# Optimization experiments

Hardware: AMD Instinct MI355X
Metric: run time of the kernel (lower is better)

## Reference

```python
import jax, jax.numpy as jnp
import numpy as np

B, H, W, D, K = 64, 32, 32, 512, 64
EPS = 1e-12


def setup_inputs() -> dict:
    key = jax.random.key(0)
    k1, k2, k3 = jax.random.split(key, 3)
    inputs = jax.random.normal(k1, (B, H, W, D), dtype=jnp.float32)
    # 1x1 conv kernel (no bias) -> equivalent to a [D, K] matmul per pixel
    w = jax.random.normal(k2, (D, K), dtype=jnp.float32) * 0.02
    # cluster centers, stored in the original as (1,1,1,D,K); we keep [D, K]
    C = jax.random.normal(k3, (D, K), dtype=jnp.float32) * 0.02
    return {"inputs": inputs, "w": w, "C": C}


def _l2norm(v, axis=-1):
    return v / jnp.sqrt(jnp.sum(v * v, axis=axis, keepdims=True) + EPS)


def reference(inputs, w, C):
    # soft-assignment: 1x1 conv + softmax over clusters
    s = jnp.einsum('bhwd,dk->bhwk', inputs, w)          # [B,H,W,K]
    a = jax.nn.softmax(s, axis=-1)
    b, h, ww, d = inputs.shape
    k = w.shape[1]
    a2 = a.reshape(b, h * ww, k)                         # [B,N,K]
    x2 = inputs.reshape(b, h * ww, d)                    # [B,N,D]
    # VLAD reformulation: sum_n a[n,k]*(x[n,d] + C[d,k])
    #  = (a^T x)[k,d] + (sum_n a[n,k]) * C[d,k]
    # avoids materializing the [B,H,W,D,K] broadcast of the original
    vkd = jnp.einsum('bnk,bnd->bkd', a2, x2)             # [B,K,D]
    vkd = vkd + a2.sum(axis=1)[:, :, None] * C.T[None]   # [B,K,D]
    # intra-normalization over D (matches transpose->normalize in original)
    vkd = _l2norm(vkd, axis=-1)
    # transpose back to [B,D,K], flatten, global L2 normalize
    v = jnp.transpose(vkd, (0, 2, 1)).reshape(b, d * k)
    v = _l2norm(v, axis=-1)
    return v
```

## Files before the change

### kernel.cpp

```cpp
#include <hip/hip_runtime.h>

#define EPS 1e-12f
typedef __attribute__((ext_vector_type(8))) short short8;
typedef __attribute__((ext_vector_type(4))) float f32x4;

__device__ __forceinline__ unsigned short f2bf(float f) {
  unsigned u = __float_as_uint(f);
  u += 0x7FFFu + ((u >> 16) & 1u);
  return (unsigned short)(u >> 16);
}
__device__ __forceinline__ float bf2f(unsigned short h) {
  return __uint_as_float(((unsigned)h) << 16);
}
__device__ __forceinline__ void split2(float f, unsigned short& h,
                                       unsigned short& l) {
  h = f2bf(f);
  l = f2bf(f - bf2f(h));
}

extern "C" __global__ __launch_bounds__(256) void netvlad_prep(
    const float* __restrict__ w, unsigned short* __restrict__ wTh,
    unsigned short* __restrict__ wTl)
{
  int tg = blockIdx.x * 256 + threadIdx.x;
  int k = tg >> 9, d = tg & 511;
  float f = w[d * 64 + k];
  unsigned short h, l;
  split2(f, h, l);
  wTh[tg] = h;
  wTl[tg] = l;
}

extern "C" __global__ __launch_bounds__(256) void netvlad_assign(
    const float* __restrict__ x, const unsigned short* __restrict__ wTh,
    const unsigned short* __restrict__ wTl, unsigned short* __restrict__ aTh,
    unsigned short* __restrict__ aTl, float* __restrict__ asum)
{
  __shared__ unsigned short xh[64 * 40];
  __shared__ unsigned short xl[64 * 40];
  __shared__ unsigned short ath[64 * 80];
  __shared__ unsigned short atl[64 * 80];
  __shared__ float asp[4 * 64];

  const int t = threadIdx.x;
  const int lane = t & 63, wv = t >> 6;
  const int lo4 = lane & 15, hi4 = lane >> 4;
  const int pxblk = blockIdx.x << 6;
  const int b = blockIdx.x >> 4;
  const int nblk = (blockIdx.x & 15) << 6;

  f32x4 acc[4] = {{0.f, 0.f, 0.f, 0.f}, {0.f, 0.f, 0.f, 0.f},
                  {0.f, 0.f, 0.f, 0.f}, {0.f, 0.f, 0.f, 0.f}};

  const int spx = t >> 2;
  const int sd = (t & 3) * 8;
  const float* xrow = x + (size_t)(pxblk + spx) * 512 + sd;

  for (int d0 = 0; d0 < 512; d0 += 32) {
    __syncthreads();
    float4 v0 = *(const float4*)(xrow + d0);
    float4 v1 = *(const float4*)(xrow + d0 + 4);
    ushort4 h0, h1, l0, l1;
    split2(v0.x, h0.x, l0.x); split2(v0.y, h0.y, l0.y);
    split2(v0.z, h0.z, l0.z); split2(v0.w, h0.w, l0.w);
    split2(v1.x, h1.x, l1.x); split2(v1.y, h1.y, l1.y);
    split2(v1.z, h1.z, l1.z); split2(v1.w, h1.w, l1.w);
    *(ushort4*)&xh[spx * 40 + sd] = h0;
    *(ushort4*)&xh[spx * 40 + sd + 4] = h1;
    *(ushort4*)&xl[spx * 40 + sd] = l0;
    *(ushort4*)&xl[spx * 40 + sd + 4] = l1;
    __syncthreads();

    short8 xfh = *(short8*)&xh[(wv * 16 + lo4) * 40 + hi4 * 8];
    short8 xfl = *(short8*)&xl[(wv * 16 + lo4) * 40 + hi4 * 8];
#pragma unroll
    for (int nt = 0; nt < 4; ++nt) {
      const size_t wo = (size_t)(nt * 16 + lo4) * 512 + d0 + hi4 * 8;
      short8 wfh = *(const short8*)(wTh + wo);
      short8 wfl = *(const short8*)(wTl + wo);
      acc[nt] = __builtin_amdgcn_mfma_f32_16x16x32_bf16(xfh, wfh, acc[nt], 0, 0, 0);
      acc[nt] = __builtin_amdgcn_mfma_f32_16x16x32_bf16(xfl, wfh, acc[nt], 0, 0, 0);
      acc[nt] = __builtin_amdgcn_mfma_f32_16x16x32_bf16(xfh, wfl, acc[nt], 0, 0, 0);
    }
  }

  float asum_p[4] = {0.f, 0.f, 0.f, 0.f};
#pragma unroll
  for (int r = 0; r < 4; ++r) {
    float s0 = acc[0][r], s1 = acc[1][r], s2 = acc[2][r], s3 = acc[3][r];
    float m = fmaxf(fmaxf(s0, s1), fmaxf(s2, s3));
    m = fmaxf(m, __shfl_xor(m, 1));
    m = fmaxf(m, __shfl_xor(m, 2));
    m = fmaxf(m, __shfl_xor(m, 4));
    m = fmaxf(m, __shfl_xor(m, 8));
    float e0 = __expf(s0 - m), e1 = __expf(s1 - m);
    float e2 = __expf(s2 - m), e3 = __expf(s3 - m);
    float s = e0 + e1 + e2 + e3;
    s += __shfl_xor(s, 1);
    s += __shfl_xor(s, 2);
    s += __shfl_xor(s, 4);
    s += __shfl_xor(s, 8);
    float inv = 1.0f / s;
    e0 *= inv; e1 *= inv; e2 *= inv; e3 *= inv;
    asum_p[0] += e0; asum_p[1] += e1; asum_p[2] += e2; asum_p[3] += e3;
    const int px = wv * 16 + hi4 * 4 + r;
    unsigned short h, l;
    split2(e0, h, l); ath[(0 * 16 + lo4) * 80 + px] = h; atl[(0 * 16 + lo4) * 80 + px] = l;
    split2(e1, h, l); ath[(1 * 16 + lo4) * 80 + px] = h; atl[(1 * 16 + lo4) * 80 + px] = l;
    split2(e2, h, l); ath[(2 * 16 + lo4) * 80 + px] = h; atl[(2 * 16 + lo4) * 80 + px] = l;
    split2(e3, h, l); ath[(3 * 16 + lo4) * 80 + px] = h; atl[(3 * 16 + lo4) * 80 + px] = l;
  }
#pragma unroll
  for (int nt = 0; nt < 4; ++nt) {
    float v = asum_p[nt];
    v += __shfl_xor(v, 16);
    v += __shfl_xor(v, 32);
    if (lane < 16) asp[wv * 64 + nt * 16 + lane] = v;
  }
  __syncthreads();
  if (t < 64) {
    float s = asp[t] + asp[64 + t] + asp[128 + t] + asp[192 + t];
    atomicAdd(&asum[b * 64 + t], s);
  }
  {
    const int k = t >> 2, po = (t & 3) * 16;
    short8 h0 = *(short8*)&ath[k * 80 + po];
    short8 h1 = *(short8*)&ath[k * 80 + po + 8];
    short8 l0 = *(short8*)&atl[k * 80 + po];
    short8 l1 = *(short8*)&atl[k * 80 + po + 8];
    const size_t go = ((size_t)(b * 64 + k) << 10) + nblk + po;
    *(short8*)(aTh + go) = h0;
    *(short8*)(aTh + go + 8) = h1;
    *(short8*)(aTl + go) = l0;
    *(short8*)(aTl + go + 8) = l1;
  }
}

extern "C" __global__ __launch_bounds__(256) void netvlad_vlad(
    const float* __restrict__ x, const unsigned short* __restrict__ aTh,
    const unsigned short* __restrict__ aTl, float* __restrict__ vkd)
{
  __shared__ unsigned short xth[32 * 40];
  __shared__ unsigned short xtl[32 * 40];
  const int t = threadIdx.x;
  const int lane = t & 63, wv = t >> 6;
  const int lo4 = lane & 15, hi4 = lane >> 4;
  const int b = blockIdx.x >> 4;
  const int ds = (blockIdx.x & 15) << 5;
  const int np = (t & 15) * 2;
  const int sdd = (t >> 4) * 2;
  const float* xs = x + (size_t)b * 1024 * 512 + ds;

  f32x4 acc[2] = {{0.f, 0.f, 0.f, 0.f}, {0.f, 0.f, 0.f, 0.f}};

  for (int n0 = 0; n0 < 1024; n0 += 32) {
    __syncthreads();
    float2 u = *(const float2*)(xs + (size_t)(n0 + np) * 512 + sdd);
    float2 v = *(const float2*)(xs + (size_t)(n0 + np + 1) * 512 + sdd);
    ushort2 h0, h1, l0, l1;
    split2(u.x, h0.x, l0.x); split2(v.x, h0.y, l0.y);
    split2(u.y, h1.x, l1.x); split2(v.y, h1.y, l1.y);
    *(ushort2*)&xth[sdd * 40 + np] = h0;
    *(ushort2*)&xth[(sdd + 1) * 40 + np] = h1;
    *(ushort2*)&xtl[sdd * 40 + np] = l0;
    *(ushort2*)&xtl[(sdd + 1) * 40 + np] = l1;
    __syncthreads();

    const size_t ao = (size_t)(b * 64 + wv * 16 + lo4) * 1024 + n0 + hi4 * 8;
    short8 ah = *(const short8*)(aTh + ao);
    short8 al = *(const short8*)(aTl + ao);
#pragma unroll
    for (int dt = 0; dt < 2; ++dt) {
      short8 bh = *(short8*)&xth[(dt * 16 + lo4) * 40 + hi4 * 8];
      short8 bl = *(short8*)&xtl[(dt * 16 + lo4) * 40 + hi4 * 8];
      acc[dt] = __builtin_amdgcn_mfma_f32_16x16x32_bf16(ah, bh, acc[dt], 0, 0, 0);
      acc[dt] = __builtin_amdgcn_mfma_f32_16x16x32_bf16(ah, bl, acc[dt], 0, 0, 0);
      acc[dt] = __builtin_amdgcn_mfma_f32_16x16x32_bf16(al, bh, acc[dt], 0, 0, 0);
    }
  }
#pragma unroll
  for (int dt = 0; dt < 2; ++dt) {
    float* vb = vkd + ((size_t)(b * 512 + ds + dt * 16 + lo4)) * 64
              + wv * 16 + hi4 * 4;
    *(float4*)vb = make_float4(acc[dt][0], acc[dt][1], acc[dt][2], acc[dt][3]);
  }
}

extern "C" __global__ __launch_bounds__(256) void netvlad_fin1(
    const float* __restrict__ vkd, const float* __restrict__ Cm,
    const float* __restrict__ asum, float* __restrict__ out,
    float* __restrict__ r_buf)
{
  __shared__ float rp[4 * 64];
  const int t = threadIdx.x;
  const int k = t & 63;
  const int dg = t >> 6;
  const int b = blockIdx.x >> 2;
  const int dq = blockIdx.x & 3;
  const float asv = asum[b * 64 + k];
  const int dbase = dq * 128 + dg * 32;
  const float* p0 = vkd + (size_t)b * 512 * 64;
  float* ob = out + (size_t)b * 512 * 64;
  float racc = 0.f;
  for (int dd = 0; dd < 32; ++dd) {
    size_t off = (size_t)(dbase + dd) * 64 + k;
    float v = p0[off] + asv * Cm[off];
    ob[off] = v;
    racc = fmaf(v, v, racc);
  }
  rp[dg * 64 + k] = racc;
  __syncthreads();
  if (t < 64) {
    float r = rp[t] + rp[64 + t] + rp[128 + t] + rp[192 + t];
    atomicAdd(&r_buf[b * 64 + t], r);
  }
}

extern "C" __global__ __launch_bounds__(64) void netvlad_fin2(
    const float* __restrict__ r_buf, float* __restrict__ scale_buf)
{
  const int b = blockIdx.x;
  const int k = threadIdx.x;
  float r = r_buf[b * 64 + k];
  float g = r / (r + EPS);
  g += __shfl_xor(g, 1);
  g += __shfl_xor(g, 2);
  g += __shfl_xor(g, 4);
  g += __shfl_xor(g, 8);
  g += __shfl_xor(g, 16);
  g += __shfl_xor(g, 32);
  scale_buf[b * 64 + k] = 1.0f / (sqrtf(r + EPS) * sqrtf(g + EPS));
}

extern "C" __global__ __launch_bounds__(256) void netvlad_fin3(
    float* __restrict__ out, const float* __restrict__ scale_buf)
{
  __shared__ float sc[64];
  const int t = threadIdx.x;
  const int b = blockIdx.x >> 3;
  if (t < 64) sc[t] = scale_buf[b * 64 + t];
  __syncthreads();
  float4* o4 = (float4*)out;
#pragma unroll
  for (int c = 0; c < 4; ++c) {
    int idx = blockIdx.x * 1024 + c * 256 + t;
    float4 v = o4[idx];
    int k4 = (idx & 15) * 4;
    v.x *= sc[k4]; v.y *= sc[k4 + 1]; v.z *= sc[k4 + 2]; v.w *= sc[k4 + 3];
    o4[idx] = v;
  }
}

extern "C" void kernel_launch(void* const* d_in, const int* in_sizes, int n_in,
                              void* d_out, int out_size, void* d_ws,
                              size_t ws_size, hipStream_t stream)
{
  const float* x  = (const float*)d_in[0];
  const float* w  = (const float*)d_in[1];
  const float* Cm = (const float*)d_in[2];
  float* out = (float*)d_out;

  unsigned short* aTh = (unsigned short*)d_ws;
  unsigned short* aTl = aTh + 4194304;
  float* vkd = (float*)(aTl + 4194304);
  unsigned short* wTh = (unsigned short*)(vkd + 2097152);
  unsigned short* wTl = wTh + 32768;
  float* asum = (float*)(wTl + 32768);
  float* r_buf = asum + 4096;
  float* scale_buf = r_buf + 4096;

  hipMemsetAsync(asum, 0, 2 * 4096 * sizeof(float), stream);

  netvlad_prep  <<< 128, 256, 0, stream>>>(w, wTh, wTl);
  netvlad_assign<<<1024, 256, 0, stream>>>(x, wTh, wTl, aTh, aTl, asum);
  netvlad_vlad  <<<1024, 256, 0, stream>>>(x, aTh, aTl, vkd);
  netvlad_fin1  <<< 256, 256, 0, stream>>>(vkd, Cm, asum, out, r_buf);
  netvlad_fin2  <<<  64,  64, 0, stream>>>(r_buf, scale_buf);
  netvlad_fin3  <<< 512, 256, 0, stream>>>(out, scale_buf);
}
```

Measured before the change: 306.0 us.

## Enlarge assign and vlad tiles, load x fragments directly, stage fp32 x in LDS

The assign kernel now handles 128 pixels per block. Each wave loads its x fragments straight from global memory into registers, with no LDS staging and no barriers in the K loop, and reuses each W fragment across two pixel tiles. The vlad kernel now covers 64 d-columns per block and all 64 clusters per wave. It stages raw fp32 x in LDS and does the bf16 hi/lo split after a transposed read, reusing each split x fragment across four cluster tiles. This halves the grid sizes and raises register pressure and LDS bank-conflict risk, in exchange for fewer barriers and more reuse of each loaded operand.

```diff
diff --git a/kernel.cpp b/kernel.cpp
--- a/kernel.cpp
+++ b/kernel.cpp
@@ -4,18 +4,37 @@
 typedef __attribute__((ext_vector_type(8))) short short8;
 typedef __attribute__((ext_vector_type(4))) float f32x4;
 
-__device__ __forceinline__ unsigned short f2bf(float f) {
-  unsigned u = __float_as_uint(f);
-  u += 0x7FFFu + ((u >> 16) & 1u);
-  return (unsigned short)(u >> 16);
-}
-__device__ __forceinline__ float bf2f(unsigned short h) {
-  return __uint_as_float(((unsigned)h) << 16);
-}
-__device__ __forceinline__ void split2(float f, unsigned short& h,
-                                       unsigned short& l) {
-  h = f2bf(f);
-  l = f2bf(f - bf2f(h));
+#define MFMA(a, b, c) __builtin_amdgcn_mfma_f32_16x16x32_bf16(a, b, c, 0, 0, 0)
+
+__device__ __forceinline__ unsigned rne16(unsigned u) {
+  return u + 0x7FFFu + ((u >> 16) & 1u);
+}
+__device__ __forceinline__ void split_pair(float f0, float f1,
+                                           unsigned& hp, unsigned& lp) {
+  unsigned u0 = __float_as_uint(f0), u1 = __float_as_uint(f1);
+  unsigned r0 = rne16(u0), r1 = rne16(u1);
+  float h0 = __uint_as_float(r0 & 0xFFFF0000u);
+  float h1 = __uint_as_float(r1 & 0xFFFF0000u);
+  hp = (r0 >> 16) | (r1 & 0xFFFF0000u);
+  unsigned v0 = rne16(__float_as_uint(f0 - h0));
+  unsigned v1 = rne16(__float_as_uint(f1 - h1));
+  lp = (v0 >> 16) | (v1 & 0xFFFF0000u);
+}
+__device__ __forceinline__ void split8(float4 a, float4 b, short8& h, short8& l) {
+  union { unsigned u[4]; short8 s; } H, L;
+  split_pair(a.x, a.y, H.u[0], L.u[0]);
+  split_pair(a.z, a.w, H.u[1], L.u[1]);
+  split_pair(b.x, b.y, H.u[2], L.u[2]);
+  split_pair(b.z, b.w, H.u[3], L.u[3]);
+  h = H.s; l = L.s;
+}
+__device__ __forceinline__ void split8f(const float* f, short8& h, short8& l) {
+  union { unsigned u[4]; short8 s; } H, L;
+  split_pair(f[0], f[1], H.u[0], L.u[0]);
+  split_pair(f[2], f[3], H.u[1], L.u[1]);
+  split_pair(f[4], f[5], H.u[2], L.u[2]);
+  split_pair(f[6], f[7], H.u[3], L.u[3]);
+  h = H.s; l = L.s;
 }
 
 extern "C" __global__ __launch_bounds__(256) void netvlad_prep(
@@ -25,10 +44,12 @@
   int tg = blockIdx.x * 256 + threadIdx.x;
   int k = tg >> 9, d = tg & 511;
   float f = w[d * 64 + k];
-  unsigned short h, l;
-  split2(f, h, l);
-  wTh[tg] = h;
-  wTl[tg] = l;
+  unsigned u = __float_as_uint(f);
+  unsigned rh = rne16(u);
+  float hf = __uint_as_float(rh & 0xFFFF0000u);
+  unsigned rl = rne16(__float_as_uint(f - hf));
+  wTh[tg] = (unsigned short)(rh >> 16);
+  wTl[tg] = (unsigned short)(rl >> 16);
 }
 
 extern "C" __global__ __launch_bounds__(256) void netvlad_assign(
@@ -36,103 +57,105 @@
     const unsigned short* __restrict__ wTl, unsigned short* __restrict__ aTh,
     unsigned short* __restrict__ aTl, float* __restrict__ asum)
 {
-  __shared__ unsigned short xh[64 * 40];
-  __shared__ unsigned short xl[64 * 40];
-  __shared__ unsigned short ath[64 * 80];
-  __shared__ unsigned short atl[64 * 80];
+  __shared__ unsigned short ath[64 * 136];
+  __shared__ unsigned short atl[64 * 136];
   __shared__ float asp[4 * 64];
 
   const int t = threadIdx.x;
   const int lane = t & 63, wv = t >> 6;
   const int lo4 = lane & 15, hi4 = lane >> 4;
-  const int pxblk = blockIdx.x << 6;
-  const int b = blockIdx.x >> 4;
-  const int nblk = (blockIdx.x & 15) << 6;
-
-  f32x4 acc[4] = {{0.f, 0.f, 0.f, 0.f}, {0.f, 0.f, 0.f, 0.f},
-                  {0.f, 0.f, 0.f, 0.f}, {0.f, 0.f, 0.f, 0.f}};
-
-  const int spx = t >> 2;
-  const int sd = (t & 3) * 8;
-  const float* xrow = x + (size_t)(pxblk + spx) * 512 + sd;
+  const int b = blockIdx.x >> 3;
+  const int nblk = (blockIdx.x & 7) << 7;
+
+  f32x4 acc[2][4] = {};
+
+  const float* xp0 =
+      x + (size_t)((blockIdx.x << 7) + (wv << 5) + lo4) * 512 + (hi4 << 3);
 
   for (int d0 = 0; d0 < 512; d0 += 32) {
-    __syncthreads();
-    float4 v0 = *(const float4*)(xrow + d0);
-    float4 v1 = *(const float4*)(xrow + d0 + 4);
-    ushort4 h0, h1, l0, l1;
-    split2(v0.x, h0.x, l0.x); split2(v0.y, h0.y, l0.y);
-    split2(v0.z, h0.z, l0.z); split2(v0.w, h0.w, l0.w);
-    split2(v1.x, h1.x, l1.x); split2(v1.y, h1.y, l1.y);
-    split2(v1.z, h1.z, l1.z); split2(v1.w, h1.w, l1.w);
-    *(ushort4*)&xh[spx * 40 + sd] = h0;
-    *(ushort4*)&xh[spx * 40 + sd + 4] = h1;
-    *(ushort4*)&xl[spx * 40 + sd] = l0;
-    *(ushort4*)&xl[spx * 40 + sd + 4] = l1;
-    __syncthreads();
-
-    short8 xfh = *(short8*)&xh[(wv * 16 + lo4) * 40 + hi4 * 8];
-    short8 xfl = *(short8*)&xl[(wv * 16 + lo4) * 40 + hi4 * 8];
+    short8 xh[2], xl[2];
+#pragma unroll
+    for (int pt = 0; pt < 2; ++pt) {
+      const float* p = xp0 + (size_t)pt * (16 * 512) + d0;
+      float4 v0 = *(const float4*)p;
+      float4 v1 = *(const float4*)(p + 4);
+      split8(v0, v1, xh[pt], xl[pt]);
+    }
 #pragma unroll
     for (int nt = 0; nt < 4; ++nt) {
-      const size_t wo = (size_t)(nt * 16 + lo4) * 512 + d0 + hi4 * 8;
-      short8 wfh = *(const short8*)(wTh + wo);
-      short8 wfl = *(const short8*)(wTl + wo);
-      acc[nt] = __builtin_amdgcn_mfma_f32_16x16x32_bf16(xfh, wfh, acc[nt], 0, 0, 0);
-      acc[nt] = __builtin_amdgcn_mfma_f32_16x16x32_bf16(xfl, wfh, acc[nt], 0, 0, 0);
-      acc[nt] = __builtin_amdgcn_mfma_f32_16x16x32_bf16(xfh, wfl, acc[nt], 0, 0, 0);
+      const size_t wo = (size_t)((nt << 4) + lo4) * 512 + d0 + (hi4 << 3);
+      short8 wh = *(const short8*)(wTh + wo);
+      short8 wl = *(const short8*)(wTl + wo);
+#pragma unroll
+      for (int pt = 0; pt < 2; ++pt) {
+        acc[pt][nt] = MFMA(xh[pt], wh, acc[pt][nt]);
+        acc[pt][nt] = MFMA(xl[pt], wh, acc[pt][nt]);
+        acc[pt][nt] = MFMA(xh[pt], wl, acc[pt][nt]);
+      }
     }
   }
 
   float asum_p[4] = {0.f, 0.f, 0.f, 0.f};
 #pragma unroll
-  for (int r = 0; r < 4; ++r) {
-    float s0 = acc[0][r], s1 = acc[1][r], s2 = acc[2][r], s3 = acc[3][r];
-    float m = fmaxf(fmaxf(s0, s1), fmaxf(s2, s3));
-    m = fmaxf(m, __shfl_xor(m, 1));
-    m = fmaxf(m, __shfl_xor(m, 2));
-    m = fmaxf(m, __shfl_xor(m, 4));
-    m = fmaxf(m, __shfl_xor(m, 8));
-    float e0 = __expf(s0 - m), e1 = __expf(s1 - m);
-    float e2 = __expf(s2 - m), e3 = __expf(s3 - m);
-    float s = e0 + e1 + e2 + e3;
-    s += __shfl_xor(s, 1);
-    s += __shfl_xor(s, 2);
-    s += __shfl_xor(s, 4);
-    s += __shfl_xor(s, 8);
-    float inv = 1.0f / s;
-    e0 *= inv; e1 *= inv; e2 *= inv; e3 *= inv;
-    asum_p[0] += e0; asum_p[1] += e1; asum_p[2] += e2; asum_p[3] += e3;
-    const int px = wv * 16 + hi4 * 4 + r;
-    unsigned short h, l;
-    split2(e0, h, l); ath[(0 * 16 + lo4) * 80 + px] = h; atl[(0 * 16 + lo4) * 80 + px] = l;
-    split2(e1, h, l); ath[(1 * 16 + lo4) * 80 + px] = h; atl[(1 * 16 + lo4) * 80 + px] = l;
-    split2(e2, h, l); ath[(2 * 16 + lo4) * 80 + px] = h; atl[(2 * 16 + lo4) * 80 + px] = l;
-    split2(e3, h, l); ath[(3 * 16 + lo4) * 80 + px] = h; atl[(3 * 16 + lo4) * 80 + px] = l;
-  }
+  for (int pt = 0; pt < 2; ++pt) {
+#pragma unroll
+    for (int r = 0; r < 4; ++r) {
+      float s0 = acc[pt][0][r], s1 = acc[pt][1][r];
+      float s2 = acc[pt][2][r], s3 = acc[pt][3][r];
+      float m = fmaxf(fmaxf(s0, s1), fmaxf(s2, s3));
+      m = fmaxf(m, __shfl_xor(m, 1));
+      m = fmaxf(m, __shfl_xor(m, 2));
+      m = fmaxf(m, __shfl_xor(m, 4));
+      m = fmaxf(m, __shfl_xor(m, 8));
+      float e0 = __expf(s0 - m), e1 = __expf(s1 - m);
+      float e2 = __expf(s2 - m), e3 = __expf(s3 - m);
+      float s = e0 + e1 + e2 + e3;
+      s += __shfl_xor(s, 1);
+      s += __shfl_xor(s, 2);
+      s += __shfl_xor(s, 4);
+      s += __shfl_xor(s, 8);
+      float inv = 1.0f / s;
+      e0 *= inv; e1 *= inv; e2 *= inv; e3 *= inv;
+      asum_p[0] += e0; asum_p[1] += e1; asum_p[2] += e2; asum_p[3] += e3;
+      acc[pt][0][r] = e0; acc[pt][1][r] = e1;
+      acc[pt][2][r] = e2; acc[pt][3][r] = e3;
+    }
+  }
+#pragma unroll
+  for (int pt = 0; pt < 2; ++pt)
+#pragma unroll
+    for (int nt = 0; nt < 4; ++nt)
+#pragma unroll
+      for (int r = 0; r < 4; ++r) {
+        float a = acc[pt][nt][r];
+        unsigned u = __float_as_uint(a);
+        unsigned rh = rne16(u);
+        float hf = __uint_as_float(rh & 0xFFFF0000u);
+        unsigned rl = rne16(__float_as_uint(a - hf));
+        int idx = ((nt << 4) + lo4) * 136 + (wv << 5) + (pt << 4) + (hi4 << 2) + r;
+        ath[idx] = (unsigned short)(rh >> 16);
+        atl[idx] = (unsigned short)(rl >> 16);
+      }
 #pragma unroll
   for (int nt = 0; nt < 4; ++nt) {
     float v = asum_p[nt];
     v += __shfl_xor(v, 16);
     v += __shfl_xor(v, 32);
-    if (lane < 16) asp[wv * 64 + nt * 16 + lane] = v;
+    if (lane < 16) asp[(wv << 6) + (nt << 4) + lane] = v;
   }
   __syncthreads();
   if (t < 64) {
     float s = asp[t] + asp[64 + t] + asp[128 + t] + asp[192 + t];
-    atomicAdd(&asum[b * 64 + t], s);
+    atomicAdd(&asum[(b << 6) + t], s);
   }
   {
-    const int k = t >> 2, po = (t & 3) * 16;
-    short8 h0 = *(short8*)&ath[k * 80 + po];
-    short8 h1 = *(short8*)&ath[k * 80 + po + 8];
-    short8 l0 = *(short8*)&atl[k * 80 + po];
-    short8 l1 = *(short8*)&atl[k * 80 + po + 8];
-    const size_t go = ((size_t)(b * 64 + k) << 10) + nblk + po;
-    *(short8*)(aTh + go) = h0;
-    *(short8*)(aTh + go + 8) = h1;
-    *(short8*)(aTl + go) = l0;
-    *(short8*)(aTl + go + 8) = l1;
+    const int k = t >> 2, px0 = (t & 3) << 5;
+    const size_t go = ((size_t)((b << 6) + k) << 10) + nblk + px0;
+#pragma unroll
+    for (int c = 0; c < 4; ++c) {
+      *(short8*)(aTh + go + (c << 3)) = *(short8*)&ath[k * 136 + px0 + (c << 3)];
+      *(short8*)(aTl + go + (c << 3)) = *(short8*)&atl[k * 136 + px0 + (c << 3)];
+    }
   }
 }
 
@@ -140,49 +163,57 @@
     const float* __restrict__ x, const unsigned short* __restrict__ aTh,
     const unsigned short* __restrict__ aTl, float* __restrict__ vkd)
 {
-  __shared__ unsigned short xth[32 * 40];
-  __shared__ unsigned short xtl[32 * 40];
+  __shared__ float xt[64 * 68];
   const int t = threadIdx.x;
   const int lane = t & 63, wv = t >> 6;
   const int lo4 = lane & 15, hi4 = lane >> 4;
-  const int b = blockIdx.x >> 4;
-  const int ds = (blockIdx.x & 15) << 5;
-  const int np = (t & 15) * 2;
-  const int sdd = (t >> 4) * 2;
-  const float* xs = x + (size_t)b * 1024 * 512 + ds;
-
-  f32x4 acc[2] = {{0.f, 0.f, 0.f, 0.f}, {0.f, 0.f, 0.f, 0.f}};
-
-  for (int n0 = 0; n0 < 1024; n0 += 32) {
+  const int b = blockIdx.x >> 3;
+  const int ds = (blockIdx.x & 7) << 6;
+  const int srow = t >> 2, scol = (t & 3) << 4;
+  const float* xs = x + ((size_t)(b << 10)) * 512 + ds;
+
+  f32x4 acc[4] = {};
+
+  for (int n0 = 0; n0 < 1024; n0 += 64) {
     __syncthreads();
-    float2 u = *(const float2*)(xs + (size_t)(n0 + np) * 512 + sdd);
-    float2 v = *(const float2*)(xs + (size_t)(n0 + np + 1) * 512 + sdd);
-    ushort2 h0, h1, l0, l1;
-    split2(u.x, h0.x, l0.x); split2(v.x, h0.y, l0.y);
-    split2(u.y, h1.x, l1.x); split2(v.y, h1.y, l1.y);
-    *(ushort2*)&xth[sdd * 40 + np] = h0;
-    *(ushort2*)&xth[(sdd + 1) * 40 + np] = h1;
-    *(ushort2*)&xtl[sdd * 40 + np] = l0;
-    *(ushort2*)&xtl[(sdd + 1) * 40 + np] = l1;
+    {
+      const float* p = xs + (size_t)(n0 + srow) * 512 + scol;
+      float4 v0 = ((const float4*)p)[0];
+      float4 v1 = ((const float4*)p)[1];
+      float4 v2 = ((const float4*)p)[2];
+      float4 v3 = ((const float4*)p)[3];
+      float* dst = &xt[srow * 68 + scol];
+      ((float4*)dst)[0] = v0;
+      ((float4*)dst)[1] = v1;
+      ((float4*)dst)[2] = v2;
+      ((float4*)dst)[3] = v3;
+    }
     __syncthreads();
-
-    const size_t ao = (size_t)(b * 64 + wv * 16 + lo4) * 1024 + n0 + hi4 * 8;
-    short8 ah = *(const short8*)(aTh + ao);
-    short8 al = *(const short8*)(aTl + ao);
-#pragma unroll
-    for (int dt = 0; dt < 2; ++dt) {
-      short8 bh = *(short8*)&xth[(dt * 16 + lo4) * 40 + hi4 * 8];
-      short8 bl = *(short8*)&xtl[(dt * 16 + lo4) * 40 + hi4 * 8];
-      acc[dt] = __builtin_amdgcn_mfma_f32_16x16x32_bf16(ah, bh, acc[dt], 0, 0, 0);
-      acc[dt] = __builtin_amdgcn_mfma_f32_16x16x32_bf16(ah, bl, acc[dt], 0, 0, 0);
-      acc[dt] = __builtin_amdgcn_mfma_f32_16x16x32_bf16(al, bh, acc[dt], 0, 0, 0);
-    }
-  }
-#pragma unroll
-  for (int dt = 0; dt < 2; ++dt) {
-    float* vb = vkd + ((size_t)(b * 512 + ds + dt * 16 + lo4)) * 64
-              + wv * 16 + hi4 * 4;
-    *(float4*)vb = make_float4(acc[dt][0], acc[dt][1], acc[dt][2], acc[dt][3]);
+#pragma unroll
+    for (int nf = 0; nf < 2; ++nf) {
+      float f[8];
+#pragma unroll
+      for (int j = 0; j < 8; ++j)
+        f[j] = xt[((nf << 5) + (hi4 << 3) + j) * 68 + (wv << 4) + lo4];
+      short8 bh, bl;
+      split8f(f, bh, bl);
+#pragma unroll
+      for (int kt = 0; kt < 4; ++kt) {
+        const size_t ao = ((size_t)((b << 6) + (kt << 4) + lo4) << 10)
+                        + n0 + (nf << 5) + (hi4 << 3);
+        short8 ah = *(const short8*)(aTh + ao);
+        short8 al = *(const short8*)(aTl + ao);
+        acc[kt] = MFMA(ah, bh, acc[kt]);
+        acc[kt] = MFMA(ah, bl, acc[kt]);
+        acc[kt] = MFMA(al, bh, acc[kt]);
+      }
+    }
+  }
+#pragma unroll
+  for (int kt = 0; kt < 4; ++kt) {
+    float* vb = vkd + (((size_t)(b << 9) + ds + (wv << 4) + lo4) << 6)
+              + (kt << 4) + (hi4 << 2);
+    *(float4*)vb = make_float4(acc[kt][0], acc[kt][1], acc[kt][2], acc[kt][3]);
   }
 }
 
@@ -271,10 +302,10 @@
 
   hipMemsetAsync(asum, 0, 2 * 4096 * sizeof(float), stream);
 
-  netvlad_prep  <<< 128, 256, 0, stream>>>(w, wTh, wTl);
-  netvlad_assign<<<1024, 256, 0, stream>>>(x, wTh, wTl, aTh, aTl, asum);
-  netvlad_vlad  <<<1024, 256, 0, stream>>>(x, aTh, aTl, vkd);
-  netvlad_fin1  <<< 256, 256, 0, stream>>>(vkd, Cm, asum, out, r_buf);
-  netvlad_fin2  <<<  64,  64, 0, stream>>>(r_buf, scale_buf);
-  netvlad_fin3  <<< 512, 256, 0, stream>>>(out, scale_buf);
-}
+  netvlad_prep  <<<128, 256, 0, stream>>>(w, wTh, wTl);
+  netvlad_assign<<<512, 256, 0, stream>>>(x, wTh, wTl, aTh, aTl, asum);
+  netvlad_vlad  <<<512, 256, 0, stream>>>(x, aTh, aTl, vkd);
+  netvlad_fin1  <<<256, 256, 0, stream>>>(vkd, Cm, asum, out, r_buf);
+  netvlad_fin2  <<< 64,  64, 0, stream>>>(r_buf, scale_buf);
+  netvlad_fin3  <<<512, 256, 0, stream>>>(out, scale_buf);
+}
```

After: 306.5 us. No clear change (+0.2%).
